# Optimization experiments

Measured on AMD Instinct MI355X. Metric: run time of the kernel, lower is better.

The kernel has to match this reference:

```python
import jax, jax.numpy as jnp
import numpy as np

# so(3) generators (3x3x3), L[s, r, a]
L = jnp.array([[[0, 0, 0], [0, 0, -1], [0, 1, 0]],
               [[0, 0, 1], [0, 0, 0], [-1, 0, 0]],
               [[0, -1, 0], [1, 0, 0], [0, 0, 0]]], dtype=jnp.float32)


def setup_inputs() -> dict:
    key = jax.random.key(0)
    B, S, X, Y = 32, 3, 512, 512
    s = jax.random.normal(key, (B, S, X, Y), dtype=jnp.float32)
    # normalize to unit O(3) spins (physically realistic; math identical for any s)
    s = s / jnp.linalg.norm(s, axis=1, keepdims=True)
    t = jnp.ones((1,), dtype=jnp.float32)   # flow time
    c0 = jnp.ones((1,), dtype=jnp.float32)  # learnable coefficient C[0]
    return {"s": s, "t": t, "c0": c0}


def reference(s, t, c0):
    # Psi11t.grad(s, t): flow force of the (psi_1^1)^2 action term.
    # Coeff(t) with EvenOdd=False and cc=[c0] is t * c0.
    coeff = t * c0  # shape [1], broadcasts

    def nbr(x, mu):
        # sum of forward and backward periodic neighbors along lattice axis mu
        return jnp.roll(x, -1, axis=mu) + jnp.roll(x, 1, axis=mu)

    # b[b,x,y] = sum_mu s . (s shifted +/- along mu)
    b = (jnp.einsum('bsxy,bsxy->bxy', s, nbr(s, 2))
         + jnp.einsum('bsxy,bsxy->bxy', s, nbr(s, 3)))

    bs = s * b[:, None]  # [B,3,X,Y]

    # Lsig[b,r,a,x,y] = -sum_s s[b,s,x,y] * L[s,r,a]
    Lsig = -jnp.einsum('bsxy,sra->braxy', s, L)

    Fs = nbr(s, 2) + nbr(s, 3)      # [B,3,X,Y]
    Fbs = nbr(bs, 2) + nbr(bs, 3)   # [B,3,X,Y]

    F = Fs * b[:, None] + Fbs
    F = jnp.einsum('bsaxy,bsxy->baxy', Lsig, F)  # so(3) generator contraction
    return 2.0 * coeff * F
```

## Files before the change

kernel.cpp:

```cpp
#include <hip/hip_runtime.h>

#define NX 512
#define NY 512
#define XY (NX * NY)

typedef float f4 __attribute__((ext_vector_type(4)));

__global__ __launch_bounds__(512, 6) void psi11t_kernel(
    const float* __restrict__ s,
    const float* __restrict__ t,
    const float* __restrict__ c0,
    float* __restrict__ out)
{
    __shared__ __align__(16) float s_lds[3 * 6 * NY];
    __shared__ __align__(16) float b_lds[6 * NY];

    const int D = blockIdx.x;
    const int L = (D & 7) * 512 + (D >> 3);
    const int bidx  = L >> 7;
    const int strip = L & 127;
    const int x0  = strip * 4;
    const int tid = threadIdx.x;
    const int y4g = tid & 127;
    const int yb  = y4g * 4;

    const float* sb = s + (size_t)bidx * 3 * XY;

    auto ldchunk = [&](int k) -> f4 {
        const int rl = k >> 7;
        const int c  = rl / 6;
        const int r  = rl - 6 * c;
        const int xg = (x0 - 1 + r) & (NX - 1);
        return *(const f4*)(sb + (size_t)c * XY + (size_t)xg * NY + (k & 127) * 4);
    };
    f4 st0 = ldchunk(tid);
    f4 st1 = ldchunk(tid + 512);
    f4 st2 = ldchunk(tid + 1024);
    f4 st3 = ldchunk(tid + 1536);
    f4 st4;
    if (tid < 256) st4 = ldchunk(tid + 2048);

    f4 ge[3];
    if (tid < 256) {
        const int xe = (tid < 128) ? ((x0 - 2) & (NX - 1)) : ((x0 + 5) & (NX - 1));
        const float* re = sb + (size_t)xe * NY + yb;
        #pragma unroll
        for (int c = 0; c < 3; ++c) ge[c] = *(const f4*)(re + (size_t)c * XY);
    }

    *(f4*)&s_lds[(size_t)tid * 4]          = st0;
    *(f4*)&s_lds[(size_t)(tid + 512) * 4]  = st1;
    *(f4*)&s_lds[(size_t)(tid + 1024) * 4] = st2;
    *(f4*)&s_lds[(size_t)(tid + 1536) * 4] = st3;
    if (tid < 256) *(f4*)&s_lds[(size_t)(tid + 2048) * 4] = st4;
    __syncthreads();

    const int ym = (yb + NY - 1) & (NY - 1);
    const int yp = (yb + 4) & (NY - 1);

    {
        const int rb = tid >> 7;
        f4 acc = {0.f, 0.f, 0.f, 0.f};
        #pragma unroll
        for (int c = 0; c < 3; ++c) {
            const float* Sc = &s_lds[(c * 6 + rb) * NY];
            f4 ce = *(const f4*)(Sc + yb);
            f4 up;
            if (rb == 0) up = ge[c];
            else         up = *(const f4*)(Sc - NY + yb);
            f4 dn = *(const f4*)(Sc + NY + yb);
            float lf = Sc[ym], rt = Sc[yp];
            f4 shl = {lf, ce[0], ce[1], ce[2]};
            f4 shr = {ce[1], ce[2], ce[3], rt};
            acc += ce * (up + dn + shl + shr);
        }
        *(f4*)&b_lds[rb * NY + yb] = acc;
    }
    if (tid < 256) {
        const int rb = 4 + (tid >> 7);
        f4 acc = {0.f, 0.f, 0.f, 0.f};
        #pragma unroll
        for (int c = 0; c < 3; ++c) {
            const float* Sc = &s_lds[(c * 6 + rb) * NY];
            f4 ce = *(const f4*)(Sc + yb);
            f4 up = *(const f4*)(Sc - NY + yb);
            f4 dn;
            if (rb == 5) dn = ge[c];
            else         dn = *(const f4*)(Sc + NY + yb);
            float lf = Sc[ym], rt = Sc[yp];
            f4 shl = {lf, ce[0], ce[1], ce[2]};
            f4 shr = {ce[1], ce[2], ce[3], rt};
            acc += ce * (up + dn + shl + shr);
        }
        *(f4*)&b_lds[rb * NY + yb] = acc;
    }
    __syncthreads();

    const int r = tid >> 7;
    const int x = x0 + r;

    const float* Bc = &b_lds[(r + 1) * NY];
    f4 bc = *(const f4*)(Bc + yb);
    f4 bu = *(const f4*)(Bc - NY + yb);
    f4 bd = *(const f4*)(Bc + NY + yb);
    float bl = Bc[ym], br = Bc[yp];
    f4 bshl = {bl, bc[0], bc[1], bc[2]};
    f4 bshr = {bc[1], bc[2], bc[3], br};

    f4 G[3], cen[3];
    #pragma unroll
    for (int c = 0; c < 3; ++c) {
        const float* Sc = &s_lds[(c * 6 + r + 1) * NY];
        f4 ce = *(const f4*)(Sc + yb);
        f4 up = *(const f4*)(Sc - NY + yb);
        f4 dn = *(const f4*)(Sc + NY + yb);
        float lf = Sc[ym], rt = Sc[yp];
        f4 shl = {lf, ce[0], ce[1], ce[2]};
        f4 shr = {ce[1], ce[2], ce[3], rt};
        f4 Fs = up + dn + shl + shr;
        G[c] = Fs * bc + up * bu + dn * bd + shl * bshl + shr * bshr;
        cen[c] = ce;
    }

    const float coeff = 2.0f * t[0] * c0[0];
    f4 o0 = (cen[1] * G[2] - cen[2] * G[1]) * coeff;
    f4 o1 = (cen[2] * G[0] - cen[0] * G[2]) * coeff;
    f4 o2 = (cen[0] * G[1] - cen[1] * G[0]) * coeff;

    float* ob = out + (size_t)bidx * 3 * XY + (size_t)x * NY + yb;
    __builtin_nontemporal_store(o0, (f4*)ob);
    __builtin_nontemporal_store(o1, (f4*)(ob + XY));
    __builtin_nontemporal_store(o2, (f4*)(ob + 2 * XY));
}

extern "C" void kernel_launch(void* const* d_in, const int* in_sizes, int n_in,
                              void* d_out, int out_size, void* d_ws, size_t ws_size,
                              hipStream_t stream) {
    const float* s  = (const float*)d_in[0];
    const float* t  = (const float*)d_in[1];
    const float* c0 = (const float*)d_in[2];
    float* out = (float*)d_out;

    psi11t_kernel<<<4096, 512, 0, stream>>>(s, t, c0, out);
}
```

Baseline: 179.5 us.

## Make kernel persistent with register prefetch of next strip's halo loads

Launches a fixed grid of 768 blocks that each loop over 5-6 consecutive strips, keeping the XCD-aware mapping. The global loads for the next strip are issued into registers before the second barrier, so they overlap with the current strip's b-stencil and output computation. Centre-row stencil values are kept in registers between the b and G phases instead of being re-read from shared memory. The trade-off is higher register pressure, which may lower occupancy, and a serialized per-block loop.

```diff
diff --git a/kernel.cpp b/kernel.cpp
--- a/kernel.cpp
+++ b/kernel.cpp
@@ -15,122 +15,141 @@
     __shared__ __align__(16) float s_lds[3 * 6 * NY];
     __shared__ __align__(16) float b_lds[6 * NY];
 
-    const int D = blockIdx.x;
-    const int L = (D & 7) * 512 + (D >> 3);
-    const int bidx  = L >> 7;
-    const int strip = L & 127;
-    const int x0  = strip * 4;
     const int tid = threadIdx.x;
-    const int y4g = tid & 127;
-    const int yb  = y4g * 4;
+    const int yb  = (tid & 127) * 4;
+    const int r   = tid >> 7;
+    const int ybm = (yb + NY - 4) & (NY - 1);
+    const int ybp = (yb + 4) & (NY - 1);
+    const bool lo256 = (tid < 256);
 
-    const float* sb = s + (size_t)bidx * 3 * XY;
-
-    auto ldchunk = [&](int k) -> f4 {
+    int sc[5], sr[5], sy[5];
+    #pragma unroll
+    for (int q = 0; q < 5; ++q) {
+        const int k  = tid + q * 512;
         const int rl = k >> 7;
         const int c  = rl / 6;
-        const int r  = rl - 6 * c;
-        const int xg = (x0 - 1 + r) & (NX - 1);
-        return *(const f4*)(sb + (size_t)c * XY + (size_t)xg * NY + (k & 127) * 4);
-    };
-    f4 st0 = ldchunk(tid);
-    f4 st1 = ldchunk(tid + 512);
-    f4 st2 = ldchunk(tid + 1024);
-    f4 st3 = ldchunk(tid + 1536);
-    f4 st4;
-    if (tid < 256) st4 = ldchunk(tid + 2048);
-
-    f4 ge[3];
-    if (tid < 256) {
-        const int xe = (tid < 128) ? ((x0 - 2) & (NX - 1)) : ((x0 + 5) & (NX - 1));
-        const float* re = sb + (size_t)xe * NY + yb;
-        #pragma unroll
-        for (int c = 0; c < 3; ++c) ge[c] = *(const f4*)(re + (size_t)c * XY);
+        sc[q] = c;
+        sr[q] = rl - 6 * c;
+        sy[q] = (k & 127) * 4;
     }
 
-    *(f4*)&s_lds[(size_t)tid * 4]          = st0;
-    *(f4*)&s_lds[(size_t)(tid + 512) * 4]  = st1;
-    *(f4*)&s_lds[(size_t)(tid + 1024) * 4] = st2;
-    *(f4*)&s_lds[(size_t)(tid + 1536) * 4] = st3;
-    if (tid < 256) *(f4*)&s_lds[(size_t)(tid + 2048) * 4] = st4;
-    __syncthreads();
+    const int xcd = blockIdx.x & 7;
+    const int j   = blockIdx.x >> 3;
+    const int cnt = (j < 32) ? 6 : 5;
+    const int g0  = xcd * 512 + ((j < 32) ? 6 * j : 192 + 5 * (j - 32));
 
-    const int ym = (yb + NY - 1) & (NY - 1);
-    const int yp = (yb + 4) & (NY - 1);
+    const float coeff = 2.0f * t[0] * c0[0];
+
+    f4 st[5], ge[3];
 
     {
-        const int rb = tid >> 7;
-        f4 acc = {0.f, 0.f, 0.f, 0.f};
+        const int bo = (g0 >> 7) * 3;
+        const int x0 = (g0 & 127) * 4;
+        #pragma unroll
+        for (int q = 0; q < 4; ++q) {
+            const int xg = (x0 - 1 + sr[q]) & (NX - 1);
+            st[q] = *(const f4*)(s + (size_t)(bo + sc[q]) * XY + (size_t)xg * NY + sy[q]);
+        }
+        if (lo256) {
+            const int xg4 = (x0 - 1 + sr[4]) & (NX - 1);
+            st[4] = *(const f4*)(s + (size_t)(bo + sc[4]) * XY + (size_t)xg4 * NY + sy[4]);
+            const int xe = (tid < 128) ? ((x0 - 2) & (NX - 1)) : ((x0 + 5) & (NX - 1));
+            const float* re = s + (size_t)bo * XY + (size_t)xe * NY + yb;
+            #pragma unroll
+            for (int c = 0; c < 3; ++c) ge[c] = *(const f4*)(re + (size_t)c * XY);
+        }
+    }
+
+    for (int i = 0; i < cnt; ++i) {
+        const int gid = g0 + i;
+        const int x0  = (gid & 127) * 4;
+        const int bo  = (gid >> 7) * 3;
+
+        #pragma unroll
+        for (int q = 0; q < 4; ++q)
+            *(f4*)&s_lds[(size_t)(tid + q * 512) * 4] = st[q];
+        if (lo256)
+            *(f4*)&s_lds[(size_t)(tid + 2048) * 4] = st[4];
+        __syncthreads();
+
+        f4 ce[3], up[3], dn[3], shl[3], shr[3], Fs[3];
+        f4 bc = {0.f, 0.f, 0.f, 0.f};
         #pragma unroll
         for (int c = 0; c < 3; ++c) {
-            const float* Sc = &s_lds[(c * 6 + rb) * NY];
-            f4 ce = *(const f4*)(Sc + yb);
-            f4 up;
-            if (rb == 0) up = ge[c];
-            else         up = *(const f4*)(Sc - NY + yb);
-            f4 dn = *(const f4*)(Sc + NY + yb);
-            float lf = Sc[ym], rt = Sc[yp];
-            f4 shl = {lf, ce[0], ce[1], ce[2]};
-            f4 shr = {ce[1], ce[2], ce[3], rt};
-            acc += ce * (up + dn + shl + shr);
+            const float* S1 = &s_lds[(c * 6 + r + 1) * NY];
+            up[c] = *(const f4*)&s_lds[(c * 6 + r) * NY + yb];
+            ce[c] = *(const f4*)(S1 + yb);
+            dn[c] = *(const f4*)&s_lds[(c * 6 + r + 2) * NY + yb];
+            const f4 pv = *(const f4*)(S1 + ybm);
+            const f4 nx = *(const f4*)(S1 + ybp);
+            shl[c] = f4{pv[3], ce[c][0], ce[c][1], ce[c][2]};
+            shr[c] = f4{ce[c][1], ce[c][2], ce[c][3], nx[0]};
+            Fs[c]  = up[c] + dn[c] + shl[c] + shr[c];
+            bc += ce[c] * Fs[c];
         }
-        *(f4*)&b_lds[rb * NY + yb] = acc;
+        *(f4*)&b_lds[(r + 1) * NY + yb] = bc;
+
+        if (lo256) {
+            const int rb = (tid < 128) ? 0 : 5;
+            const int ro = (tid < 128) ? 1 : 4;
+            f4 acc = {0.f, 0.f, 0.f, 0.f};
+            #pragma unroll
+            for (int c = 0; c < 3; ++c) {
+                const float* S0 = &s_lds[(c * 6 + rb) * NY];
+                const f4 c2 = *(const f4*)(S0 + yb);
+                const f4 p2 = *(const f4*)(S0 + ybm);
+                const f4 n2 = *(const f4*)(S0 + ybp);
+                const f4 ot = *(const f4*)&s_lds[(c * 6 + ro) * NY + yb];
+                const f4 sl  = {p2[3], c2[0], c2[1], c2[2]};
+                const f4 sr2 = {c2[1], c2[2], c2[3], n2[0]};
+                acc += c2 * (ge[c] + ot + sl + sr2);
+            }
+            *(f4*)&b_lds[rb * NY + yb] = acc;
+        }
+
+        if (i + 1 < cnt) {
+            const int g1  = gid + 1;
+            const int bo1 = (g1 >> 7) * 3;
+            const int x1  = (g1 & 127) * 4;
+            #pragma unroll
+            for (int q = 0; q < 4; ++q) {
+                const int xg = (x1 - 1 + sr[q]) & (NX - 1);
+                st[q] = *(const f4*)(s + (size_t)(bo1 + sc[q]) * XY + (size_t)xg * NY + sy[q]);
+            }
+            if (lo256) {
+                const int xg4 = (x1 - 1 + sr[4]) & (NX - 1);
+                st[4] = *(const f4*)(s + (size_t)(bo1 + sc[4]) * XY + (size_t)xg4 * NY + sy[4]);
+                const int xe = (tid < 128) ? ((x1 - 2) & (NX - 1)) : ((x1 + 5) & (NX - 1));
+                const float* re = s + (size_t)bo1 * XY + (size_t)xe * NY + yb;
+                #pragma unroll
+                for (int c = 0; c < 3; ++c) ge[c] = *(const f4*)(re + (size_t)c * XY);
+            }
+        }
+
+        __syncthreads();
+
+        const float* B1 = &b_lds[(r + 1) * NY];
+        const f4 bu = *(const f4*)&b_lds[r * NY + yb];
+        const f4 bd = *(const f4*)&b_lds[(r + 2) * NY + yb];
+        const f4 bp = *(const f4*)(B1 + ybm);
+        const f4 bn = *(const f4*)(B1 + ybp);
+        const f4 bshl = {bp[3], bc[0], bc[1], bc[2]};
+        const f4 bshr = {bc[1], bc[2], bc[3], bn[0]};
+
+        f4 G[3];
+        #pragma unroll
+        for (int c = 0; c < 3; ++c)
+            G[c] = Fs[c] * bc + up[c] * bu + dn[c] * bd + shl[c] * bshl + shr[c] * bshr;
+
+        const f4 o0 = (ce[1] * G[2] - ce[2] * G[1]) * coeff;
+        const f4 o1 = (ce[2] * G[0] - ce[0] * G[2]) * coeff;
+        const f4 o2 = (ce[0] * G[1] - ce[1] * G[0]) * coeff;
+
+        float* ob = out + (size_t)bo * XY + (size_t)(x0 + r) * NY + yb;
+        __builtin_nontemporal_store(o0, (f4*)ob);
+        __builtin_nontemporal_store(o1, (f4*)(ob + XY));
+        __builtin_nontemporal_store(o2, (f4*)(ob + 2 * XY));
     }
-    if (tid < 256) {
-        const int rb = 4 + (tid >> 7);
-        f4 acc = {0.f, 0.f, 0.f, 0.f};
-        #pragma unroll
-        for (int c = 0; c < 3; ++c) {
-            const float* Sc = &s_lds[(c * 6 + rb) * NY];
-            f4 ce = *(const f4*)(Sc + yb);
-            f4 up = *(const f4*)(Sc - NY + yb);
-            f4 dn;
-            if (rb == 5) dn = ge[c];
-            else         dn = *(const f4*)(Sc + NY + yb);
-            float lf = Sc[ym], rt = Sc[yp];
-            f4 shl = {lf, ce[0], ce[1], ce[2]};
-            f4 shr = {ce[1], ce[2], ce[3], rt};
-            acc += ce * (up + dn + shl + shr);
-        }
-        *(f4*)&b_lds[rb * NY + yb] = acc;
-    }
-    __syncthreads();
-
-    const int r = tid >> 7;
-    const int x = x0 + r;
-
-    const float* Bc = &b_lds[(r + 1) * NY];
-    f4 bc = *(const f4*)(Bc + yb);
-    f4 bu = *(const f4*)(Bc - NY + yb);
-    f4 bd = *(const f4*)(Bc + NY + yb);
-    float bl = Bc[ym], br = Bc[yp];
-    f4 bshl = {bl, bc[0], bc[1], bc[2]};
-    f4 bshr = {bc[1], bc[2], bc[3], br};
-
-    f4 G[3], cen[3];
-    #pragma unroll
-    for (int c = 0; c < 3; ++c) {
-        const float* Sc = &s_lds[(c * 6 + r + 1) * NY];
-        f4 ce = *(const f4*)(Sc + yb);
-        f4 up = *(const f4*)(Sc - NY + yb);
-        f4 dn = *(const f4*)(Sc + NY + yb);
-        float lf = Sc[ym], rt = Sc[yp];
-        f4 shl = {lf, ce[0], ce[1], ce[2]};
-        f4 shr = {ce[1], ce[2], ce[3], rt};
-        f4 Fs = up + dn + shl + shr;
-        G[c] = Fs * bc + up * bu + dn * bd + shl * bshl + shr * bshr;
-        cen[c] = ce;
-    }
-
-    const float coeff = 2.0f * t[0] * c0[0];
-    f4 o0 = (cen[1] * G[2] - cen[2] * G[1]) * coeff;
-    f4 o1 = (cen[2] * G[0] - cen[0] * G[2]) * coeff;
-    f4 o2 = (cen[0] * G[1] - cen[1] * G[0]) * coeff;
-
-    float* ob = out + (size_t)bidx * 3 * XY + (size_t)x * NY + yb;
-    __builtin_nontemporal_store(o0, (f4*)ob);
-    __builtin_nontemporal_store(o1, (f4*)(ob + XY));
-    __builtin_nontemporal_store(o2, (f4*)(ob + 2 * XY));
 }
 
 extern "C" void kernel_launch(void* const* d_in, const int* in_sizes, int n_in,
@@ -141,5 +160,5 @@
     const float* c0 = (const float*)d_in[2];
     float* out = (float*)d_out;
 
-    psi11t_kernel<<<4096, 512, 0, stream>>>(s, t, c0, out);
+    psi11t_kernel<<<768, 512, 0, stream>>>(s, t, c0, out);
 }
```

Result: slower. 312.1 us (+73.9%).
